# Performance work log

Hardware: AMD Instinct MI355X
Metric: run time of the kernel (lower is better)

The kernel has to match this reference:

```python
import jax, jax.numpy as jnp
import numpy as np

N_VISIBLE = 50000
N_HIDDEN = 5000
N_NODES = N_VISIBLE + N_HIDDEN
N_EDGES = 1_000_000
BATCH = 128


def setup_inputs() -> dict:
    key = jax.random.key(0)
    k1, k2, k3, k4, k5 = jax.random.split(key, 5)
    # parameters, initialized as in the torch module
    linear = 0.05 * (2.0 * jax.random.uniform(k1, (N_NODES,), dtype=jnp.float32) - 1.0)
    quadratic = 5.0 * (2.0 * jax.random.uniform(k2, (N_EDGES,), dtype=jnp.float32) - 1.0)
    # bipartite visible-hidden edges -> CSR-like flat buffers (via segment ids)
    flat_adj = jax.random.randint(k3, (N_EDGES,), 0, N_VISIBLE, dtype=jnp.int32).astype(jnp.int64)  # visible endpoint per edge
    seg_ids = jax.random.randint(k4, (N_EDGES,), 0, N_HIDDEN, dtype=jnp.int32).astype(jnp.int64)    # hidden bin per edge
    flat_j_idx = jnp.arange(N_EDGES, dtype=jnp.int64)  # quadratic coefficient index per flat entry
    hidden_idx = jnp.arange(N_HIDDEN, dtype=jnp.int64) + N_VISIBLE
    # observed spin configurations in {0,1} (mapped to +-1 inside reference)
    s = jax.random.randint(k5, (BATCH, N_NODES), 0, 2, dtype=jnp.int32)
    return {
        "linear": linear,
        "quadratic": quadratic,
        "s": s,
        "flat_adj": flat_adj,
        "flat_j_idx": flat_j_idx,
        "seg_ids": seg_ids,
        "hidden_idx": hidden_idx,
        "n_hidden": N_HIDDEN,
    }


def reference(linear, quadratic, s, flat_adj, flat_j_idx, seg_ids, hidden_idx, n_hidden):
    """Per-hidden-unit effective field + conditional spin expectation.

    eff[b, k] = linear[hidden_idx[k]]
                + sum_{e : seg_ids[e]==k} quadratic[flat_j_idx[e]] * s_pm[b, flat_adj[e]]
    returns tanh(-eff)  (conditional expectation of hidden spins given visibles)
    """
    s_pm = (2 * s - 1).astype(linear.dtype)                 # {0,1} -> {-1,+1}, (B, N)
    w = quadratic[flat_j_idx]                               # (E,)
    contrib = s_pm[:, flat_adj].T * w[:, None]              # (E, B) gathered neighbor terms
    field = jax.ops.segment_sum(contrib, seg_ids, num_segments=n_hidden)  # (K, B)
    eff = field.T + linear[hidden_idx][None, :]             # (B, K)
    return jnp.tanh(-eff)
```

## Files before the change

kernel.cpp:

```cpp
#include <hip/hip_runtime.h>
#include <math.h>
#include <stdint.h>

#define NV 50000
#define NH 5000
#define NN 55000
#define NCB 157
#define BCAP 8192
#define FSLOT 384
#define CHUNK 2048


__global__ void __launch_bounds__(256) pack_zero_kernel(
        const int* __restrict__ s, uint32_t* __restrict__ bits,
        uint32_t* __restrict__ coarse_cnt) {
    if (blockIdx.x == 0 && threadIdx.x < NCB) coarse_cnt[threadIdx.x] = 0u;
    int tid = blockIdx.x * 256 + threadIdx.x;
    int v = tid >> 2;
    int g = tid & 3;
    if (v >= NV) return;
    const int* col = s + (size_t)g * 32 * NN + v;
    uint32_t w = 0;
#pragma unroll
    for (int j = 0; j < 32; ++j)
        w |= (uint32_t)(col[(size_t)j * NN] & 1) << j;
    bits[(size_t)v * 4 + g] = w;
}

__global__ void __launch_bounds__(256) coarse_split_kernel(
        const int4* __restrict__ seg4, const int4* __restrict__ adj4,
        const float4* __restrict__ quad4,
        uint32_t* __restrict__ coarse_cnt, uint2* __restrict__ recs, int E) {
    __shared__ uint32_t hist[NCB];
    __shared__ uint32_t loc[NCB];
    __shared__ uint32_t gbase[NCB];
    __shared__ __align__(16) uint2 st[CHUNK];
    __shared__ uint32_t std_[CHUNK];
    const int tid = threadIdx.x;
    for (int i = tid; i < NCB; i += 256) hist[i] = 0u;
    __syncthreads();

    const int c0 = blockIdx.x * CHUNK;
    const int nloc = min(CHUNK, E - c0);
    int kreg[CHUNK / 1024 * 4];
#pragma unroll
    for (int j = 0; j < CHUNK / 1024; ++j) {
        int t4 = (c0 >> 2) + j * 256 + tid;
        bool ok = (t4 * 4) < (c0 + nloc);
        int4 sg = ok ? seg4[t4] : make_int4(-1, -1, -1, -1);
        kreg[j * 4 + 0] = sg.x; kreg[j * 4 + 1] = sg.y;
        kreg[j * 4 + 2] = sg.z; kreg[j * 4 + 3] = sg.w;
        if (ok) {
            atomicAdd(&hist[sg.x >> 5], 1u);
            atomicAdd(&hist[sg.y >> 5], 1u);
            atomicAdd(&hist[sg.z >> 5], 1u);
            atomicAdd(&hist[sg.w >> 5], 1u);
        }
    }
    __syncthreads();
    if (tid < NCB) gbase[tid] = atomicAdd(&coarse_cnt[tid], hist[tid]);
    __syncthreads();
    if (tid == 0) {
        uint32_t run = 0;
        for (int b = 0; b < NCB; ++b) { loc[b] = run; run += hist[b]; }
        for (int b = 0; b < NCB; ++b) hist[b] = loc[b];
    }
    __syncthreads();
#pragma unroll
    for (int j = 0; j < CHUNK / 1024; ++j) {
        int t4 = (c0 >> 2) + j * 256 + tid;
        if ((t4 * 4) < (c0 + nloc)) {
            int4 a = adj4[t4];
            float4 q = quad4[t4];
#pragma unroll
            for (int cmp = 0; cmp < 4; ++cmp) {
                int k = kreg[j * 4 + cmp];
                int v = (cmp == 0) ? a.x : (cmp == 1) ? a.y : (cmp == 2) ? a.z : a.w;
                float w = (cmp == 0) ? q.x : (cmp == 1) ? q.y : (cmp == 2) ? q.z : q.w;
                int b = k >> 5;
                uint32_t slot = atomicAdd(&hist[b], 1u);
                uint32_t rank = gbase[b] + (slot - loc[b]);
                st[slot] = make_uint2((uint32_t)v | ((uint32_t)(k & 31) << 16),
                                      __float_as_uint(w));
                std_[slot] = (rank < BCAP) ? (uint32_t)b * BCAP + rank : ~0u;
            }
        }
    }
    __syncthreads();
    for (int i = tid; i < nloc; i += 256) {
        uint32_t d = std_[i];
        if (d != ~0u) recs[d] = st[i];
    }
}

__global__ void __launch_bounds__(256) fine_sort_kernel(
        const uint32_t* __restrict__ coarse_cnt, uint2* __restrict__ recs,
        uint32_t* __restrict__ cnt_k, uint32_t* __restrict__ koff) {
    const int b = blockIdx.x;
    __shared__ __align__(16) uint2 st[BCAP];
    __shared__ uint16_t ord[BCAP];
    __shared__ uint32_t hist[32], off[32], cur[32];
    const int tid = threadIdx.x;
    if (tid < 32) hist[tid] = 0u;
    __syncthreads();
    int cnt = (int)min(coarse_cnt[b], (uint32_t)BCAP);
    uint2* region = recs + (size_t)b * BCAP;
    for (int i = tid; i < cnt; i += 256) {
        uint2 r = region[i];
        st[i] = r;
        atomicAdd(&hist[(r.x >> 16) & 31], 1u);
    }
    __syncthreads();
    if (tid == 0) {
        uint32_t run = 0;
        for (int j = 0; j < 32; ++j) { off[j] = run; cur[j] = run; run += hist[j]; }
    }
    __syncthreads();
    for (int i = tid; i < cnt; i += 256) {
        uint32_t kl = (st[i].x >> 16) & 31;
        uint32_t r = atomicAdd(&cur[kl], 1u);
        ord[r] = (uint16_t)i;
    }
    __syncthreads();
    for (int i = tid; i < cnt; i += 256) region[i] = st[ord[i]];
    if (tid < 32) {
        int k = b * 32 + tid;
        if (k < NH) { cnt_k[k] = hist[tid]; koff[k] = (uint32_t)b * BCAP + off[tid]; }
    }
}

__global__ void __launch_bounds__(256) field_tanh_kernel(
        const uint32_t* __restrict__ cnt_k, const uint32_t* __restrict__ koff,
        const uint2* __restrict__ recs, const uint4* __restrict__ bits4,
        const float* __restrict__ linear, float* __restrict__ out) {
    int g8 = blockIdx.x & 7;
    int m = blockIdx.x >> 3;
    int pair = m + 313 * g8;
    if (pair >= NH / 2) return;
    int k0 = pair * 2;
    int tid = threadIdx.x;

    __shared__ __align__(16) uint32_t rows[2][5][FSLOT];
    __shared__ float part[2][256];

    int T8s[2];
#pragma unroll
    for (int kk = 0; kk < 2; ++kk) {
        int k = k0 + kk;
        int T = (int)cnt_k[k];
        if (T > FSLOT) T = FSLOT;
        const uint2* base = recs + koff[k];
        int T8 = (T + 7) & ~7;
        T8s[kk] = T8;
        for (int i = T + tid; i < T8; i += 256) rows[kk][4][i] = 0u;
        for (int t = tid; t < T; t += 256) {
            uint2 r = base[t];
            uint4 mw = bits4[r.x & 0xFFFFu];
            rows[kk][0][t] = mw.x;
            rows[kk][1][t] = mw.y;
            rows[kk][2][t] = mw.z;
            rows[kk][3][t] = mw.w;
            rows[kk][4][t] = r.y;
        }
    }
    __syncthreads();

    int b = tid & 127;
    int grp = tid >> 7;
    const int bsh = b & 31;
    const int widx = b >> 5;
#pragma unroll
    for (int kk = 0; kk < 2; ++kk) {
        const uint32_t* mrow = rows[kk][widx];
        const uint32_t* wrow = rows[kk][4];
        float a0 = 0.f, a1 = 0.f, a2 = 0.f, a3 = 0.f;
        for (int i = grp * 4; i < T8s[kk]; i += 8) {
            uint4 mm = *(const uint4*)(mrow + i);
            uint4 ww = *(const uint4*)(wrow + i);
            float f0 = __uint_as_float(ww.x);
            float f1 = __uint_as_float(ww.y);
            float f2 = __uint_as_float(ww.z);
            float f3 = __uint_as_float(ww.w);
            a0 += ((mm.x >> bsh) & 1u) ? f0 : -f0;
            a1 += ((mm.y >> bsh) & 1u) ? f1 : -f1;
            a2 += ((mm.z >> bsh) & 1u) ? f2 : -f2;
            a3 += ((mm.w >> bsh) & 1u) ? f3 : -f3;
        }
        part[kk][tid] = (a0 + a1) + (a2 + a3);
    }
    __syncthreads();
    if (tid < 128) {
        float e0 = part[0][tid] + part[0][tid + 128] + linear[NV + k0];
        float e1 = part[1][tid] + part[1][tid + 128] + linear[NV + k0 + 1];
        float2 o = make_float2(tanhf(-e0), tanhf(-e1));
        *(float2*)(out + (size_t)tid * NH + k0) = o;
    }
}

extern "C" void kernel_launch(void* const* d_in, const int* in_sizes, int n_in,
                              void* d_out, int out_size, void* d_ws, size_t ws_size,
                              hipStream_t stream) {
    const float* linear = (const float*)d_in[0];
    const float* quad   = (const float*)d_in[1];
    const int*   s      = (const int*)d_in[2];
    const int*   adj    = (const int*)d_in[3];
    const int*   seg    = (const int*)d_in[5];
    const int E = in_sizes[5];
    float* out = (float*)d_out;

    char* ws = (char*)d_ws;
    uint32_t* bits       = (uint32_t*)(ws);
    uint32_t* coarse_cnt = (uint32_t*)(ws + 800000);
    uint32_t* cnt_k      = (uint32_t*)(ws + 800640);
    uint32_t* koff       = (uint32_t*)(ws + 820640);
    uint2*    recs       = (uint2*)   (ws + 840704);

    pack_zero_kernel<<<(NV * 4 + 255) / 256, 256, 0, stream>>>(s, bits, coarse_cnt);
    const int nchunk = (E + CHUNK - 1) / CHUNK;
    coarse_split_kernel<<<nchunk, 256, 0, stream>>>(
        (const int4*)seg, (const int4*)adj, (const float4*)quad, coarse_cnt, recs, E);
    fine_sort_kernel<<<NCB, 256, 0, stream>>>(coarse_cnt, recs, cnt_k, koff);
    field_tanh_kernel<<<313 * 8, 256, 0, stream>>>(cnt_k, koff, recs, (const uint4*)bits,
                                                   linear, out);
}
```

Baseline: 151.3 us.

## Fuse fine sort with field/tanh into one per-bucket kernel, 16-unit buckets

Fuses the fine sort and the field/tanh stages into a single kernel. Each of 313 blocks sorts its bucket of 16 hidden units in shared memory and computes their fields four units at a time. This removes one launch and a global write/read of the sorted records. The coarse split now uses 16-unit buckets, 4096-edge chunks and a parallel shared-memory scan in place of the single-thread prefix sum. The cost is only 313 blocks of 512 threads with large shared memory, which may underfill the GPU compared with the previous 2504-block field kernel.

Result: faster. 146.9 us (-2.9%).

```diff
diff --git a/kernel.cpp b/kernel.cpp
--- a/kernel.cpp
+++ b/kernel.cpp
@@ -5,16 +5,18 @@
 #define NV 50000
 #define NH 5000
 #define NN 55000
-#define NCB 157
-#define BCAP 8192
+#define NCB 313
+#define BCAP 4096
 #define FSLOT 384
-#define CHUNK 2048
+#define CHUNK 4096
+#define SCAN_N 320
 
 
 __global__ void __launch_bounds__(256) pack_zero_kernel(
         const int* __restrict__ s, uint32_t* __restrict__ bits,
         uint32_t* __restrict__ coarse_cnt) {
-    if (blockIdx.x == 0 && threadIdx.x < NCB) coarse_cnt[threadIdx.x] = 0u;
+    if (blockIdx.x == 0)
+        for (int i = threadIdx.x; i < NCB; i += 256) coarse_cnt[i] = 0u;
     int tid = blockIdx.x * 256 + threadIdx.x;
     int v = tid >> 2;
     int g = tid & 3;
@@ -31,45 +33,54 @@
         const int4* __restrict__ seg4, const int4* __restrict__ adj4,
         const float4* __restrict__ quad4,
         uint32_t* __restrict__ coarse_cnt, uint2* __restrict__ recs, int E) {
-    __shared__ uint32_t hist[NCB];
-    __shared__ uint32_t loc[NCB];
+    __shared__ uint32_t hist[SCAN_N];
+    __shared__ uint32_t loc[SCAN_N];
+    __shared__ uint32_t cur[NCB];
     __shared__ uint32_t gbase[NCB];
     __shared__ __align__(16) uint2 st[CHUNK];
-    __shared__ uint32_t std_[CHUNK];
+    __shared__ uint32_t dst[CHUNK];
     const int tid = threadIdx.x;
-    for (int i = tid; i < NCB; i += 256) hist[i] = 0u;
+    for (int i = tid; i < SCAN_N; i += 256) hist[i] = 0u;
     __syncthreads();
 
     const int c0 = blockIdx.x * CHUNK;
     const int nloc = min(CHUNK, E - c0);
-    int kreg[CHUNK / 1024 * 4];
-#pragma unroll
-    for (int j = 0; j < CHUNK / 1024; ++j) {
+    int kreg[16];
+#pragma unroll
+    for (int j = 0; j < 4; ++j) {
         int t4 = (c0 >> 2) + j * 256 + tid;
-        bool ok = (t4 * 4) < (c0 + nloc);
+        bool ok = t4 < ((c0 + nloc) >> 2);
         int4 sg = ok ? seg4[t4] : make_int4(-1, -1, -1, -1);
         kreg[j * 4 + 0] = sg.x; kreg[j * 4 + 1] = sg.y;
         kreg[j * 4 + 2] = sg.z; kreg[j * 4 + 3] = sg.w;
         if (ok) {
-            atomicAdd(&hist[sg.x >> 5], 1u);
-            atomicAdd(&hist[sg.y >> 5], 1u);
-            atomicAdd(&hist[sg.z >> 5], 1u);
-            atomicAdd(&hist[sg.w >> 5], 1u);
-        }
-    }
-    __syncthreads();
-    if (tid < NCB) gbase[tid] = atomicAdd(&coarse_cnt[tid], hist[tid]);
-    __syncthreads();
-    if (tid == 0) {
-        uint32_t run = 0;
-        for (int b = 0; b < NCB; ++b) { loc[b] = run; run += hist[b]; }
-        for (int b = 0; b < NCB; ++b) hist[b] = loc[b];
-    }
-    __syncthreads();
-#pragma unroll
-    for (int j = 0; j < CHUNK / 1024; ++j) {
+            atomicAdd(&hist[sg.x >> 4], 1u);
+            atomicAdd(&hist[sg.y >> 4], 1u);
+            atomicAdd(&hist[sg.z >> 4], 1u);
+            atomicAdd(&hist[sg.w >> 4], 1u);
+        }
+    }
+    __syncthreads();
+    for (int i = tid; i < NCB; i += 256)
+        gbase[i] = atomicAdd(&coarse_cnt[i], hist[i]);
+    for (int i = tid; i < SCAN_N; i += 256) loc[i] = hist[i];
+    __syncthreads();
+    for (int d = 1; d < SCAN_N; d <<= 1) {
+        uint32_t v0 = 0, v1 = 0;
+        int i1 = tid + 256;
+        if (tid >= d) v0 = loc[tid - d];
+        if (i1 < SCAN_N && i1 >= d) v1 = loc[i1 - d];
+        __syncthreads();
+        if (tid >= d) loc[tid] += v0;
+        if (i1 < SCAN_N && i1 >= d) loc[i1] += v1;
+        __syncthreads();
+    }
+    for (int i = tid; i < NCB; i += 256) cur[i] = loc[i] - hist[i];
+    __syncthreads();
+#pragma unroll
+    for (int j = 0; j < 4; ++j) {
         int t4 = (c0 >> 2) + j * 256 + tid;
-        if ((t4 * 4) < (c0 + nloc)) {
+        if (t4 < ((c0 + nloc) >> 2)) {
             int4 a = adj4[t4];
             float4 q = quad4[t4];
 #pragma unroll
@@ -77,123 +88,113 @@
                 int k = kreg[j * 4 + cmp];
                 int v = (cmp == 0) ? a.x : (cmp == 1) ? a.y : (cmp == 2) ? a.z : a.w;
                 float w = (cmp == 0) ? q.x : (cmp == 1) ? q.y : (cmp == 2) ? q.z : q.w;
-                int b = k >> 5;
-                uint32_t slot = atomicAdd(&hist[b], 1u);
-                uint32_t rank = gbase[b] + (slot - loc[b]);
-                st[slot] = make_uint2((uint32_t)v | ((uint32_t)(k & 31) << 16),
+                int bk = k >> 4;
+                uint32_t slot = atomicAdd(&cur[bk], 1u);
+                uint32_t rank = gbase[bk] + (slot - (loc[bk] - hist[bk]));
+                st[slot] = make_uint2((uint32_t)v | ((uint32_t)(k & 15) << 16),
                                       __float_as_uint(w));
-                std_[slot] = (rank < BCAP) ? (uint32_t)b * BCAP + rank : ~0u;
+                dst[slot] = (rank < BCAP) ? (uint32_t)bk * BCAP + rank : ~0u;
             }
         }
     }
     __syncthreads();
     for (int i = tid; i < nloc; i += 256) {
-        uint32_t d = std_[i];
+        uint32_t d = dst[i];
         if (d != ~0u) recs[d] = st[i];
     }
 }
 
-__global__ void __launch_bounds__(256) fine_sort_kernel(
-        const uint32_t* __restrict__ coarse_cnt, uint2* __restrict__ recs,
-        uint32_t* __restrict__ cnt_k, uint32_t* __restrict__ koff) {
-    const int b = blockIdx.x;
+__global__ void __launch_bounds__(512) bucket_field_kernel(
+        const uint32_t* __restrict__ coarse_cnt, const uint2* __restrict__ recs,
+        const uint4* __restrict__ bits4, const float* __restrict__ linear,
+        float* __restrict__ out) {
+    const int bkt = blockIdx.x;
+    const int tid = threadIdx.x;
+    __shared__ uint32_t hist[16], off[16], cur[16];
     __shared__ __align__(16) uint2 st[BCAP];
-    __shared__ uint16_t ord[BCAP];
-    __shared__ uint32_t hist[32], off[32], cur[32];
-    const int tid = threadIdx.x;
-    if (tid < 32) hist[tid] = 0u;
-    __syncthreads();
-    int cnt = (int)min(coarse_cnt[b], (uint32_t)BCAP);
-    uint2* region = recs + (size_t)b * BCAP;
-    for (int i = tid; i < cnt; i += 256) {
-        uint2 r = region[i];
-        st[i] = r;
-        atomicAdd(&hist[(r.x >> 16) & 31], 1u);
-    }
+    __shared__ __align__(16) uint32_t rows[4][5][FSLOT];
+    __shared__ float part[4][512];
+
+    int cnt = (int)min(coarse_cnt[bkt], (uint32_t)BCAP);
+    const uint2* region = recs + (size_t)bkt * BCAP;
+    if (tid < 16) hist[tid] = 0u;
+    __syncthreads();
+    for (int i = tid; i < cnt; i += 512)
+        atomicAdd(&hist[(region[i].x >> 16) & 15], 1u);
     __syncthreads();
     if (tid == 0) {
         uint32_t run = 0;
-        for (int j = 0; j < 32; ++j) { off[j] = run; cur[j] = run; run += hist[j]; }
-    }
-    __syncthreads();
-    for (int i = tid; i < cnt; i += 256) {
-        uint32_t kl = (st[i].x >> 16) & 31;
-        uint32_t r = atomicAdd(&cur[kl], 1u);
-        ord[r] = (uint16_t)i;
-    }
-    __syncthreads();
-    for (int i = tid; i < cnt; i += 256) region[i] = st[ord[i]];
-    if (tid < 32) {
-        int k = b * 32 + tid;
-        if (k < NH) { cnt_k[k] = hist[tid]; koff[k] = (uint32_t)b * BCAP + off[tid]; }
-    }
-}
-
-__global__ void __launch_bounds__(256) field_tanh_kernel(
-        const uint32_t* __restrict__ cnt_k, const uint32_t* __restrict__ koff,
-        const uint2* __restrict__ recs, const uint4* __restrict__ bits4,
-        const float* __restrict__ linear, float* __restrict__ out) {
-    int g8 = blockIdx.x & 7;
-    int m = blockIdx.x >> 3;
-    int pair = m + 313 * g8;
-    if (pair >= NH / 2) return;
-    int k0 = pair * 2;
-    int tid = threadIdx.x;
-
-    __shared__ __align__(16) uint32_t rows[2][5][FSLOT];
-    __shared__ float part[2][256];
-
-    int T8s[2];
-#pragma unroll
-    for (int kk = 0; kk < 2; ++kk) {
-        int k = k0 + kk;
-        int T = (int)cnt_k[k];
-        if (T > FSLOT) T = FSLOT;
-        const uint2* base = recs + koff[k];
-        int T8 = (T + 7) & ~7;
-        T8s[kk] = T8;
-        for (int i = T + tid; i < T8; i += 256) rows[kk][4][i] = 0u;
-        for (int t = tid; t < T; t += 256) {
-            uint2 r = base[t];
-            uint4 mw = bits4[r.x & 0xFFFFu];
-            rows[kk][0][t] = mw.x;
-            rows[kk][1][t] = mw.y;
-            rows[kk][2][t] = mw.z;
-            rows[kk][3][t] = mw.w;
-            rows[kk][4][t] = r.y;
-        }
-    }
-    __syncthreads();
-
-    int b = tid & 127;
-    int grp = tid >> 7;
+        for (int j = 0; j < 16; ++j) { off[j] = run; cur[j] = run; run += hist[j]; }
+    }
+    __syncthreads();
+    for (int i = tid; i < cnt; i += 512) {
+        uint2 r = region[i];
+        st[atomicAdd(&cur[(r.x >> 16) & 15], 1u)] = r;
+    }
+    __syncthreads();
+
+    const int b = tid & 127;
+    const int grp = tid >> 7;
     const int bsh = b & 31;
     const int widx = b >> 5;
-#pragma unroll
-    for (int kk = 0; kk < 2; ++kk) {
-        const uint32_t* mrow = rows[kk][widx];
-        const uint32_t* wrow = rows[kk][4];
-        float a0 = 0.f, a1 = 0.f, a2 = 0.f, a3 = 0.f;
-        for (int i = grp * 4; i < T8s[kk]; i += 8) {
-            uint4 mm = *(const uint4*)(mrow + i);
-            uint4 ww = *(const uint4*)(wrow + i);
-            float f0 = __uint_as_float(ww.x);
-            float f1 = __uint_as_float(ww.y);
-            float f2 = __uint_as_float(ww.z);
-            float f3 = __uint_as_float(ww.w);
-            a0 += ((mm.x >> bsh) & 1u) ? f0 : -f0;
-            a1 += ((mm.y >> bsh) & 1u) ? f1 : -f1;
-            a2 += ((mm.z >> bsh) & 1u) ? f2 : -f2;
-            a3 += ((mm.w >> bsh) & 1u) ? f3 : -f3;
-        }
-        part[kk][tid] = (a0 + a1) + (a2 + a3);
-    }
-    __syncthreads();
-    if (tid < 128) {
-        float e0 = part[0][tid] + part[0][tid + 128] + linear[NV + k0];
-        float e1 = part[1][tid] + part[1][tid + 128] + linear[NV + k0 + 1];
-        float2 o = make_float2(tanhf(-e0), tanhf(-e1));
-        *(float2*)(out + (size_t)tid * NH + k0) = o;
+    for (int rnd = 0; rnd < 4; ++rnd) {
+        {
+            int kk = grp;
+            int kl = rnd * 4 + kk;
+            int c = min((int)hist[kl], FSLOT);
+            int base = (int)off[kl];
+            int T16 = (c + 15) & ~15;
+            int lt = b;
+            for (int t = c + lt; t < T16; t += 128) rows[kk][4][t] = 0u;
+            for (int t = lt; t < c; t += 128) {
+                uint2 r = st[base + t];
+                uint4 mw = bits4[r.x & 0xFFFFu];
+                rows[kk][0][t] = mw.x;
+                rows[kk][1][t] = mw.y;
+                rows[kk][2][t] = mw.z;
+                rows[kk][3][t] = mw.w;
+                rows[kk][4][t] = r.y;
+            }
+        }
+        __syncthreads();
+#pragma unroll
+        for (int kk = 0; kk < 4; ++kk) {
+            int kl = rnd * 4 + kk;
+            int T16 = (min((int)hist[kl], FSLOT) + 15) & ~15;
+            const uint32_t* mrow = rows[kk][widx];
+            const uint32_t* wrow = rows[kk][4];
+            float a0 = 0.f, a1 = 0.f, a2 = 0.f, a3 = 0.f;
+            for (int i = grp * 4; i < T16; i += 16) {
+                uint4 mm = *(const uint4*)(mrow + i);
+                uint4 ww = *(const uint4*)(wrow + i);
+                float f0 = __uint_as_float(ww.x);
+                float f1 = __uint_as_float(ww.y);
+                float f2 = __uint_as_float(ww.z);
+                float f3 = __uint_as_float(ww.w);
+                a0 += ((mm.x >> bsh) & 1u) ? f0 : -f0;
+                a1 += ((mm.y >> bsh) & 1u) ? f1 : -f1;
+                a2 += ((mm.z >> bsh) & 1u) ? f2 : -f2;
+                a3 += ((mm.w >> bsh) & 1u) ? f3 : -f3;
+            }
+            part[kk][tid] = (a0 + a1) + (a2 + a3);
+        }
+        __syncthreads();
+        if (tid < 128) {
+            int k0 = bkt * 16 + rnd * 4;
+            if (k0 < NH) {
+                float4 o;
+                float* op = (float*)&o;
+#pragma unroll
+                for (int kk = 0; kk < 4; ++kk) {
+                    float e = part[kk][tid] + part[kk][tid + 128]
+                            + part[kk][tid + 256] + part[kk][tid + 384]
+                            + linear[NV + k0 + kk];
+                    op[kk] = tanhf(-e);
+                }
+                *(float4*)(out + (size_t)tid * NH + k0) = o;
+            }
+        }
+        __syncthreads();
     }
 }
 
@@ -211,15 +212,12 @@
     char* ws = (char*)d_ws;
     uint32_t* bits       = (uint32_t*)(ws);
     uint32_t* coarse_cnt = (uint32_t*)(ws + 800000);
-    uint32_t* cnt_k      = (uint32_t*)(ws + 800640);
-    uint32_t* koff       = (uint32_t*)(ws + 820640);
-    uint2*    recs       = (uint2*)   (ws + 840704);
+    uint2*    recs       = (uint2*)   (ws + 801280);
 
     pack_zero_kernel<<<(NV * 4 + 255) / 256, 256, 0, stream>>>(s, bits, coarse_cnt);
     const int nchunk = (E + CHUNK - 1) / CHUNK;
     coarse_split_kernel<<<nchunk, 256, 0, stream>>>(
         (const int4*)seg, (const int4*)adj, (const float4*)quad, coarse_cnt, recs, E);
-    fine_sort_kernel<<<NCB, 256, 0, stream>>>(coarse_cnt, recs, cnt_k, koff);
-    field_tanh_kernel<<<313 * 8, 256, 0, stream>>>(cnt_k, koff, recs, (const uint4*)bits,
-                                                   linear, out);
-}
+    bucket_field_kernel<<<NCB, 512, 0, stream>>>(coarse_cnt, recs, (const uint4*)bits,
+                                                 linear, out);
+}
```
